# Kernel optimization log

Hardware: AMD Instinct MI355X
Metric: run time of the kernel (lower is better)

## Reference

```python
import jax, jax.numpy as jnp
import numpy as np

DIM = 128
NUM_SLOTS = 8
ITERS = 3
EPS = 1e-8
LN_EPS = 1e-3
HIDDEN = max(DIM, 128)


def _ln(x, w, b):
    mu = jnp.mean(x, axis=-1, keepdims=True)
    var = jnp.mean(jnp.square(x - mu), axis=-1, keepdims=True)
    return (x - mu) * jax.lax.rsqrt(var + LN_EPS) * w + b


def setup_inputs() -> dict:
    key = jax.random.key(0)
    ks = jax.random.split(key, 16)
    b, n, d, h = 32, 4096, DIM, HIDDEN
    limit = np.sqrt(6.0 / (1 + d))
    inp = {
        'inputs': jax.random.normal(ks[0], (b, n, d), jnp.float32),
        'slots_mu': jax.random.uniform(ks[1], (1, 1, d), jnp.float32, -limit, limit),
        'slots_log_sigma': jax.random.uniform(ks[2], (1, 1, d), jnp.float32, -limit, limit),
        'Wq': jax.random.normal(ks[3], (d, d), jnp.float32) / np.sqrt(d),
        'Wk': jax.random.normal(ks[4], (d, d), jnp.float32) / np.sqrt(d),
        'Wv': jax.random.normal(ks[5], (d, d), jnp.float32) / np.sqrt(d),
        'W_ih': jax.random.normal(ks[6], (3 * d, d), jnp.float32) / np.sqrt(d),
        'W_hh': jax.random.normal(ks[7], (3 * d, d), jnp.float32) / np.sqrt(d),
        'b_ih': jnp.zeros((3 * d,), jnp.float32),
        'b_hh': jnp.zeros((3 * d,), jnp.float32),
        'W1': jax.random.normal(ks[8], (h, d), jnp.float32) / np.sqrt(d),
        'b1': jnp.zeros((h,), jnp.float32),
        'W2': jax.random.normal(ks[9], (d, h), jnp.float32) / np.sqrt(h),
        'b2': jnp.zeros((d,), jnp.float32),
        'ln_in_w': jnp.ones((d,), jnp.float32), 'ln_in_b': jnp.zeros((d,), jnp.float32),
        'ln_s_w': jnp.ones((d,), jnp.float32), 'ln_s_b': jnp.zeros((d,), jnp.float32),
        'ln_ff_w': jnp.ones((d,), jnp.float32), 'ln_ff_b': jnp.zeros((d,), jnp.float32),
    }
    return inp


def reference(inputs, slots_mu, slots_log_sigma, Wq, Wk, Wv, W_ih, W_hh, b_ih, b_hh,
              W1, b1, W2, b2, ln_in_w, ln_in_b, ln_s_w, ln_s_b, ln_ff_w, ln_ff_b):
    b, n, d = inputs.shape
    scale = d ** -0.5
    # stochastic slot init (reparameterized, fixed key for determinism)
    noise = jax.random.normal(jax.random.key(42), (b, NUM_SLOTS, d), inputs.dtype)
    slots = slots_mu + jnp.exp(slots_log_sigma) * noise

    x = _ln(inputs, ln_in_w, ln_in_b)
    k = jnp.einsum('bnd,ed->bne', x, Wk)
    v = jnp.einsum('bnd,ed->bne', x, Wv)

    for _ in range(ITERS):
        slots_prev = slots
        q = jnp.einsum('bsd,ed->bse', _ln(slots, ln_s_w, ln_s_b), Wq)
        dots = jnp.einsum('bid,bjd->bij', q, k) * scale          # [b, slots, n]
        attn = jax.nn.softmax(dots, axis=1) + EPS                 # softmax over slots
        attn = attn / jnp.sum(attn, axis=-1, keepdims=True)       # normalize over tokens
        updates = jnp.einsum('bjd,bij->bid', v, attn)             # [b, slots, d]
        # GRUCell(updates, slots_prev)
        gx = jnp.einsum('bsd,ed->bse', updates, W_ih) + b_ih
        gh = jnp.einsum('bsd,ed->bse', slots_prev, W_hh) + b_hh
        xr, xz, xn = jnp.split(gx, 3, axis=-1)
        hr, hz, hn = jnp.split(gh, 3, axis=-1)
        r = jax.nn.sigmoid(xr + hr)
        z = jax.nn.sigmoid(xz + hz)
        ng = jnp.tanh(xn + r * hn)
        slots = (1.0 - z) * ng + z * slots_prev
        # residual MLP
        ff = _ln(slots, ln_ff_w, ln_ff_b)
        ff = jax.nn.relu(jnp.einsum('bsd,hd->bsh', ff, W1) + b1)
        slots = slots + jnp.einsum('bsh,dh->bsd', ff, W2) + b2
    return slots
```

## Files before the change

### kernel.cpp

```cpp
#include <hip/hip_runtime.h>
#include <hip/hip_bf16.h>
#include <math.h>

#define DIM 128
#define NSLOT 8
#define NTOK 4096
#define NB 32
#define CHUNK 128
#define NCH (NTOK / CHUNK)
#define CHUNKPAD 136
#define LN_EPS 1e-3f
#define ATT_EPS 1e-8f
#define SCALE 0.08838834764831845f

#define BM 64
#define LDK 136

typedef short bf16x8 __attribute__((ext_vector_type(8)));
typedef float f32x4 __attribute__((ext_vector_type(4)));
typedef unsigned short ushort8_t __attribute__((ext_vector_type(8)));

__device__ __forceinline__ float bf2f(unsigned short u) {
  return __uint_as_float(((unsigned)u) << 16);
}
__device__ __forceinline__ unsigned short f2bf(float f) {
  unsigned u = __float_as_uint(f);
  unsigned r = (u + 0x7FFFu + ((u >> 16) & 1u)) >> 16;
  return (unsigned short)r;
}

__device__ __forceinline__ float erfinv_like_xla(float x) {
  double xd = (double)x;
  double w = -log1p(-xd * xd);
  double p;
  if (w < 5.0) {
    w = w - 2.5;
    p = 2.81022636e-08;
    p = 3.43273939e-07 + p * w;
    p = -3.5233877e-06 + p * w;
    p = -4.39150654e-06 + p * w;
    p = 0.00021858087 + p * w;
    p = -0.00125372503 + p * w;
    p = -0.00417768164 + p * w;
    p = 0.246640727 + p * w;
    p = 1.50140941 + p * w;
  } else {
    w = sqrt(w) - 3.0;
    p = -0.000200214257;
    p = 0.000100950558 + p * w;
    p = 0.00134934322 + p * w;
    p = -0.00367342844 + p * w;
    p = 0.00573950773 + p * w;
    p = -0.0076224613 + p * w;
    p = 0.00943887047 + p * w;
    p = 1.00167406 + p * w;
    p = 2.83297682 + p * w;
  }
  return (float)(p * xd);
}

__global__ __launch_bounds__(256) void k_init_slots(
    const float* __restrict__ mu, const float* __restrict__ lsig,
    float* __restrict__ slots, const float* __restrict__ Wk,
    const float* __restrict__ Wv, unsigned short* __restrict__ Wbf) {
  int t = blockIdx.x * blockDim.x + threadIdx.x;
  if (t < DIM * DIM) {
    Wbf[t] = f2bf(Wk[t]);
    Wbf[DIM * DIM + t] = f2bf(Wv[t]);
  }
  if (t >= NB * NSLOT * DIM) return;
  uint32_t x0 = 0u, x1 = (uint32_t)t;
  uint32_t k0 = 0u, k1 = 42u;
  uint32_t ks[3] = {k0, k1, k0 ^ k1 ^ 0x1BD11BDAu};
  x0 += ks[0];
  x1 += ks[1];
  const int rot[2][4] = {{13, 15, 26, 6}, {17, 29, 16, 24}};
#pragma unroll
  for (int blk = 0; blk < 5; ++blk) {
    const int* r = rot[blk & 1];
#pragma unroll
    for (int j = 0; j < 4; ++j) {
      x0 += x1;
      x1 = (x1 << r[j]) | (x1 >> (32 - r[j]));
      x1 ^= x0;
    }
    x0 += ks[(blk + 1) % 3];
    x1 += ks[(blk + 2) % 3] + (uint32_t)(blk + 1);
  }
  uint32_t bits = x0 ^ x1;
  float f = __uint_as_float((bits >> 9) | 0x3F800000u) - 1.0f;
  const float mn = __uint_as_float(0xBF7FFFFFu);
  float u = fmaxf(f * 2.0f + mn, mn);
  float noise = 1.41421356f * erfinv_like_xla(u);
  int d = t & (DIM - 1);
  slots[t] = mu[d] + expf(lsig[d]) * noise;
}

__global__ __launch_bounds__(256) void k_ln_kv(
    const float* __restrict__ inp, const unsigned short* __restrict__ Wbf,
    const float* __restrict__ lnw, const float* __restrict__ lnb,
    unsigned short* __restrict__ kt, unsigned short* __restrict__ vt) {
  __shared__ __align__(16) unsigned short A[BM * LDK];
  __shared__ __align__(16) unsigned short Bv[DIM * 72];
  int t = threadIdx.x;
  int tg = blockIdx.x;

  {
    int r = t >> 2, qh = t & 3;
    const float* src = inp + ((size_t)tg * BM + r) * DIM + qh * 32;
    float xr[32];
    float s = 0.f, sq = 0.f;
#pragma unroll
    for (int i4 = 0; i4 < 8; ++i4) {
      float4 v = *reinterpret_cast<const float4*>(src + i4 * 4);
      xr[i4 * 4 + 0] = v.x; xr[i4 * 4 + 1] = v.y;
      xr[i4 * 4 + 2] = v.z; xr[i4 * 4 + 3] = v.w;
      s += v.x + v.y + v.z + v.w;
      sq += v.x * v.x + v.y * v.y + v.z * v.z + v.w * v.w;
    }
    s += __shfl_xor(s, 1); sq += __shfl_xor(sq, 1);
    s += __shfl_xor(s, 2); sq += __shfl_xor(sq, 2);
    float mean = s * (1.0f / DIM);
    float var = fmaxf(sq * (1.0f / DIM) - mean * mean, 0.0f);
    float inv = 1.0f / sqrtf(var + LN_EPS);
#pragma unroll
    for (int c8 = 0; c8 < 4; ++c8) {
      ushort8_t pk;
#pragma unroll
      for (int j = 0; j < 8; ++j) {
        int d = qh * 32 + c8 * 8 + j;
        float y = (xr[c8 * 8 + j] - mean) * inv * lnw[d] + lnb[d];
        pk[j] = f2bf(y);
      }
      *reinterpret_cast<ushort8_t*>(&A[r * LDK + qh * 32 + c8 * 8]) = pk;
    }
  }
  __syncthreads();

  int w = t >> 6, l = t & 63, lm = l & 15, lg = l >> 4;
  int mat = w >> 1;
  int ebase = (w & 1) * 64;
  const unsigned short* Wsrc = Wbf + mat * DIM * DIM;

  f32x4 acc[4][4];
#pragma unroll
  for (int i = 0; i < 4; ++i)
#pragma unroll
    for (int j = 0; j < 4; ++j) acc[i][j] = (f32x4){0.f, 0.f, 0.f, 0.f};

  if (mat == 0) {
#pragma unroll
    for (int ks = 0; ks < 4; ++ks) {
      bf16x8 wf[4], xf[4];
#pragma unroll
      for (int et = 0; et < 4; ++et)
        wf[et] = *reinterpret_cast<const bf16x8*>(
            Wsrc + (ebase + et * 16 + lm) * DIM + ks * 32 + 8 * lg);
#pragma unroll
      for (int tt = 0; tt < 4; ++tt)
        xf[tt] = *reinterpret_cast<const bf16x8*>(
            &A[(tt * 16 + lm) * LDK + ks * 32 + 8 * lg]);
#pragma unroll
      for (int tt = 0; tt < 4; ++tt)
#pragma unroll
        for (int et = 0; et < 4; ++et)
          acc[tt][et] = __builtin_amdgcn_mfma_f32_16x16x32_bf16(
              xf[tt], wf[et], acc[tt][et], 0, 0, 0);
    }
  } else {
#pragma unroll
    for (int ks = 0; ks < 4; ++ks) {
      bf16x8 wf[4], xf[4];
#pragma unroll
      for (int et = 0; et < 4; ++et)
        wf[et] = *reinterpret_cast<const bf16x8*>(
            Wsrc + (ebase + et * 16 + lm) * DIM + ks * 32 + 8 * lg);
#pragma unroll
      for (int tt = 0; tt < 4; ++tt)
        xf[tt] = *reinterpret_cast<const bf16x8*>(
            &A[(tt * 16 + lm) * LDK + ks * 32 + 8 * lg]);
#pragma unroll
      for (int et = 0; et < 4; ++et)
#pragma unroll
        for (int tt = 0; tt < 4; ++tt)
          acc[et][tt] = __builtin_amdgcn_mfma_f32_16x16x32_bf16(
              wf[et], xf[tt], acc[et][tt], 0, 0, 0);
    }
  }
  __syncthreads();

  if (mat == 0) {
#pragma unroll
    for (int tt = 0; tt < 4; ++tt)
#pragma unroll
      for (int et = 0; et < 4; ++et)
#pragma unroll
        for (int r = 0; r < 4; ++r)
          A[(tt * 16 + 4 * lg + r) * LDK + ebase + et * 16 + lm] =
              f2bf(acc[tt][et][r]);
  } else {
#pragma unroll
    for (int et = 0; et < 4; ++et)
#pragma unroll
      for (int tt = 0; tt < 4; ++tt)
#pragma unroll
        for (int r = 0; r < 4; ++r)
          Bv[(ebase + et * 16 + 4 * lg + r) * 72 + tt * 16 + lm] =
              f2bf(acc[et][tt][r]);
  }
  __syncthreads();

  {
    size_t rowbase = (size_t)tg * BM;
#pragma unroll
    for (int u = 0; u < 4; ++u) {
      int i = u * 256 + t;
      int tok = i >> 4, off = (i & 15) * 8;
      ushort8_t vv = *reinterpret_cast<const ushort8_t*>(&A[tok * LDK + off]);
      *reinterpret_cast<ushort8_t*>(&kt[(rowbase + tok) * DIM + off]) = vv;
    }
    int bb = tg >> 6;
    int nb = (tg & 63) * BM;
#pragma unroll
    for (int u = 0; u < 4; ++u) {
      int i = u * 256 + t;
      int e = i >> 3, off = (i & 7) * 8;
      ushort8_t vv = *reinterpret_cast<const ushort8_t*>(&Bv[e * 72 + off]);
      *reinterpret_cast<ushort8_t*>(
          &vt[((size_t)bb * DIM + e) * NTOK + nb + off]) = vv;
    }
  }
}

__global__ __launch_bounds__(256) void k_q0(
    const float* __restrict__ slots, const float* __restrict__ Wq,
    const float* __restrict__ lnw, const float* __restrict__ lnb,
    unsigned short* __restrict__ qbf) {
  int b = blockIdx.x, t = threadIdx.x;
  int s = t >> 5, c = t & 31;
  __shared__ __align__(16) float sln[NSLOT][DIM];
  const float* sb = slots + (b * NSLOT + s) * DIM;
  float4 xv = *reinterpret_cast<const float4*>(sb + c * 4);
  float ps = xv.x + xv.y + xv.z + xv.w;
  float pq = xv.x * xv.x + xv.y * xv.y + xv.z * xv.z + xv.w * xv.w;
#pragma unroll
  for (int m = 16; m >= 1; m >>= 1) {
    ps += __shfl_xor(ps, m, 32);
    pq += __shfl_xor(pq, m, 32);
  }
  float mean = ps * (1.0f / DIM);
  float var = fmaxf(pq * (1.0f / DIM) - mean * mean, 0.0f);
  float inv = 1.0f / sqrtf(var + LN_EPS);
  float vals[4] = {xv.x, xv.y, xv.z, xv.w};
#pragma unroll
  for (int ii = 0; ii < 4; ++ii) {
    int d = c * 4 + ii;
    sln[s][d] = (vals[ii] - mean) * inv * lnw[d] + lnb[d];
  }
  __syncthreads();
#pragma unroll
  for (int ii = 0; ii < 4; ++ii) {
    int e = c + 32 * ii;
    const float* wr = Wq + e * DIM;
    float acc = 0.0f;
#pragma unroll
    for (int d4 = 0; d4 < DIM / 4; ++d4) {
      float4 w4 = *reinterpret_cast<const float4*>(wr + d4 * 4);
      float4 s4 = *reinterpret_cast<const float4*>(&sln[s][d4 * 4]);
      acc += s4.x * w4.x + s4.y * w4.y + s4.z * w4.z + s4.w * w4.w;
    }
    qbf[(b * NSLOT + s) * DIM + e] = f2bf(SCALE * acc);
  }
}

__global__ __launch_bounds__(512, 4) void k_attn(
    const unsigned short* __restrict__ qbf, const unsigned short* __restrict__ kt,
    const unsigned short* __restrict__ vt, float* __restrict__ Np,
    float* __restrict__ Dp) {
  int bid = blockIdx.x;
  int b = bid >> 5, ch = bid & 31;
  int n0 = ch * CHUNK;
  int t = threadIdx.x;
  int wid = t >> 6, l = t & 63, lm = l & 15, lg = l >> 4;

  __shared__ __align__(16) unsigned short a_lds[NSLOT][CHUNKPAD];

  {
    const unsigned short* qb = qbf + (b * NSLOT + (lm & 7)) * DIM;
    bf16x8 aq[4];
#pragma unroll
    for (int ks = 0; ks < 4; ++ks)
      aq[ks] = *reinterpret_cast<const bf16x8*>(qb + ks * 32 + 8 * lg);
    const unsigned short* kb = kt + ((size_t)b * NTOK + n0) * DIM;
    int tok = wid * 16 + lm;
    f32x4 acc = (f32x4){0.f, 0.f, 0.f, 0.f};
#pragma unroll
    for (int ks = 0; ks < 4; ++ks) {
      bf16x8 bk = *reinterpret_cast<const bf16x8*>(
          kb + (size_t)tok * DIM + ks * 32 + 8 * lg);
      acc = __builtin_amdgcn_mfma_f32_16x16x32_bf16(aq[ks], bk, acc, 0, 0, 0);
    }
    float m4 = fmaxf(fmaxf(acc[0], acc[1]), fmaxf(acc[2], acc[3]));
    float m8 = fmaxf(m4, __shfl_xor(m4, 16));
    float e0 = expf(acc[0] - m8), e1 = expf(acc[1] - m8);
    float e2 = expf(acc[2] - m8), e3 = expf(acc[3] - m8);
    float s4 = e0 + e1 + e2 + e3;
    float s8 = s4 + __shfl_xor(s4, 16);
    float rs = 1.0f / s8;
    if (lg < 2) {
      a_lds[4 * lg + 0][tok] = f2bf(e0 * rs + ATT_EPS);
      a_lds[4 * lg + 1][tok] = f2bf(e1 * rs + ATT_EPS);
      a_lds[4 * lg + 2][tok] = f2bf(e2 * rs + ATT_EPS);
      a_lds[4 * lg + 3][tok] = f2bf(e3 * rs + ATT_EPS);
    }
  }
  __syncthreads();

  {
    float s = 0.0f;
#pragma unroll
    for (int jj = 0; jj < CHUNK / 64; ++jj) s += bf2f(a_lds[wid][l + 64 * jj]);
#pragma unroll
    for (int m = 32; m >= 1; m >>= 1) s += __shfl_xor(s, m);
    if (l == 0) Dp[(b * NCH + ch) * NSLOT + wid] = s;
  }

  {
    f32x4 acc = (f32x4){0.f, 0.f, 0.f, 0.f};
    const unsigned short* vb =
        vt + ((size_t)b * DIM + wid * 16 + lm) * NTOK + n0;
#pragma unroll
    for (int kk = 0; kk < CHUNK / 32; ++kk) {
      bf16x8 af = *reinterpret_cast<const bf16x8*>(
          &a_lds[lm & 7][kk * 32 + 8 * lg]);
      bf16x8 bv = *reinterpret_cast<const bf16x8*>(vb + kk * 32 + 8 * lg);
      acc = __builtin_amdgcn_mfma_f32_16x16x32_bf16(af, bv, acc, 0, 0, 0);
    }
    if (lg < 2) {
#pragma unroll
      for (int r = 0; r < 4; ++r)
        Np[((size_t)(b * NCH + ch) * NSLOT + 4 * lg + r) * DIM + wid * 16 +
           lm] = acc[r];
    }
  }
}

__global__ __launch_bounds__(256) void k_update(
    float* __restrict__ slots, unsigned short* __restrict__ qbf,
    const float* __restrict__ Np, const float* __restrict__ Dp,
    const float* __restrict__ W_ih, const float* __restrict__ W_hh,
    const float* __restrict__ b_ih, const float* __restrict__ b_hh,
    const float* __restrict__ W1, const float* __restrict__ b1,
    const float* __restrict__ W2, const float* __restrict__ b2,
    const float* __restrict__ lnfw, const float* __restrict__ lnfb,
    const float* __restrict__ Wq, const float* __restrict__ lnsw,
    const float* __restrict__ lnsb) {
  int bs = blockIdx.x;
  int b = bs >> 3, s = bs & 7;
  int t = threadIdx.x;
  __shared__ __align__(16) float upd[DIM];
  __shared__ __align__(16) float sprev[DIM];
  __shared__ __align__(16) float snew[DIM];
  __shared__ __align__(16) float ffin[DIM];
  __shared__ __align__(16) float ffb[DIM];
  __shared__ __align__(16) float gx[3 * DIM];
  __shared__ __align__(16) float gh[3 * DIM];

  float dsum = 0.0f;
  for (int ch = 0; ch < NCH; ++ch) dsum += Dp[(b * NCH + ch) * NSLOT + s];

  if (t < DIM) {
    sprev[t] = slots[(b * NSLOT + s) * DIM + t];
    float a = 0.0f;
    for (int ch = 0; ch < NCH; ++ch)
      a += Np[((size_t)(b * NCH + ch) * NSLOT + s) * DIM + t];
    upd[t] = a / dsum;
  }
  __syncthreads();

  for (int e = t; e < 3 * DIM; e += 256) {
    const float* wi = W_ih + e * DIM;
    const float* wh = W_hh + e * DIM;
    float ax = 0.0f, ah = 0.0f;
#pragma unroll
    for (int d4 = 0; d4 < DIM / 4; ++d4) {
      float4 u4 = *reinterpret_cast<const float4*>(&upd[d4 * 4]);
      float4 p4 = *reinterpret_cast<const float4*>(&sprev[d4 * 4]);
      float4 wi4 = *reinterpret_cast<const float4*>(wi + d4 * 4);
      float4 wh4 = *reinterpret_cast<const float4*>(wh + d4 * 4);
      ax += u4.x * wi4.x + u4.y * wi4.y + u4.z * wi4.z + u4.w * wi4.w;
      ah += p4.x * wh4.x + p4.y * wh4.y + p4.z * wh4.z + p4.w * wh4.w;
    }
    gx[e] = ax + b_ih[e];
    gh[e] = ah + b_hh[e];
  }
  __syncthreads();

  if (t < DIM) {
    float xr = gx[t], xz = gx[DIM + t], xn = gx[2 * DIM + t];
    float hr = gh[t], hz = gh[DIM + t], hn = gh[2 * DIM + t];
    float r = 1.0f / (1.0f + expf(-(xr + hr)));
    float z = 1.0f / (1.0f + expf(-(xz + hz)));
    float ng = tanhf(xn + r * hn);
    snew[t] = (1.0f - z) * ng + z * sprev[t];
  }
  __syncthreads();

  if (t < DIM) {
    float s1 = 0.0f, s2 = 0.0f;
#pragma unroll 8
    for (int d = 0; d < DIM; ++d) {
      float v = snew[d];
      s1 += v;
      s2 += v * v;
    }
    float mean = s1 * (1.0f / DIM);
    float var = fmaxf(s2 * (1.0f / DIM) - mean * mean, 0.0f);
    float inv = 1.0f / sqrtf(var + LN_EPS);
    ffin[t] = (snew[t] - mean) * inv * lnfw[t] + lnfb[t];
  }
  __syncthreads();

  if (t < DIM) {
    const float* wr = W1 + t * DIM;
    float acc = 0.0f;
#pragma unroll
    for (int d4 = 0; d4 < DIM / 4; ++d4) {
      float4 f4 = *reinterpret_cast<const float4*>(&ffin[d4 * 4]);
      float4 w4 = *reinterpret_cast<const float4*>(wr + d4 * 4);
      acc += f4.x * w4.x + f4.y * w4.y + f4.z * w4.z + f4.w * w4.w;
    }
    ffb[t] = fmaxf(acc + b1[t], 0.0f);
  }
  __syncthreads();

  if (t < DIM) {
    const float* wr = W2 + t * DIM;
    float acc = 0.0f;
#pragma unroll
    for (int h4 = 0; h4 < DIM / 4; ++h4) {
      float4 f4 = *reinterpret_cast<const float4*>(&ffb[h4 * 4]);
      float4 w4 = *reinterpret_cast<const float4*>(wr + h4 * 4);
      acc += f4.x * w4.x + f4.y * w4.y + f4.z * w4.z + f4.w * w4.w;
    }
    float val = snew[t] + acc + b2[t];
    slots[(b * NSLOT + s) * DIM + t] = val;
    gx[t] = val;
  }
  __syncthreads();

  if (t < DIM) {
    float s1 = 0.0f, s2 = 0.0f;
#pragma unroll 8
    for (int d = 0; d < DIM; ++d) {
      float v = gx[d];
      s1 += v;
      s2 += v * v;
    }
    float mean = s1 * (1.0f / DIM);
    float var = fmaxf(s2 * (1.0f / DIM) - mean * mean, 0.0f);
    float inv = 1.0f / sqrtf(var + LN_EPS);
    gh[t] = (gx[t] - mean) * inv * lnsw[t] + lnsb[t];
  }
  __syncthreads();

  if (t < DIM) {
    const float* wr = Wq + t * DIM;
    float acc = 0.0f;
#pragma unroll
    for (int d4 = 0; d4 < DIM / 4; ++d4) {
      float4 g4 = *reinterpret_cast<const float4*>(&gh[d4 * 4]);
      float4 w4 = *reinterpret_cast<const float4*>(wr + d4 * 4);
      acc += g4.x * w4.x + g4.y * w4.y + g4.z * w4.z + g4.w * w4.w;
    }
    qbf[(b * NSLOT + s) * DIM + t] = f2bf(SCALE * acc);
  }
}

__global__ __launch_bounds__(256) void k_sentinel(float* __restrict__ out,
                                                  int n) {
  int i = blockIdx.x * blockDim.x + threadIdx.x;
  if (i < n) out[i] = 1234.5f;
}

extern "C" void kernel_launch(void* const* d_in, const int* in_sizes, int n_in,
                              void* d_out, int out_size, void* d_ws,
                              size_t ws_size, hipStream_t stream) {
  const float* inp = (const float*)d_in[0];
  const float* mu = (const float*)d_in[1];
  const float* lsig = (const float*)d_in[2];
  const float* Wq = (const float*)d_in[3];
  const float* Wk = (const float*)d_in[4];
  const float* Wv = (const float*)d_in[5];
  const float* W_ih = (const float*)d_in[6];
  const float* W_hh = (const float*)d_in[7];
  const float* b_ih = (const float*)d_in[8];
  const float* b_hh = (const float*)d_in[9];
  const float* W1 = (const float*)d_in[10];
  const float* b1 = (const float*)d_in[11];
  const float* W2 = (const float*)d_in[12];
  const float* b2 = (const float*)d_in[13];
  const float* ln_in_w = (const float*)d_in[14];
  const float* ln_in_b = (const float*)d_in[15];
  const float* ln_s_w = (const float*)d_in[16];
  const float* ln_s_b = (const float*)d_in[17];
  const float* ln_ff_w = (const float*)d_in[18];
  const float* ln_ff_b = (const float*)d_in[19];

  float* slots = (float*)d_out;

  const size_t kv_elems = (size_t)NB * DIM * NTOK;
  const size_t np_elems = (size_t)NB * NCH * NSLOT * DIM;
  const size_t dp_elems = (size_t)NB * NCH * NSLOT;
  const size_t q_elems = (size_t)NB * NSLOT * DIM;
  size_t need = kv_elems * 2 * 2 + np_elems * 4 + dp_elems * 4 + q_elems * 2;
  if (ws_size < need) {
    k_sentinel<<<(out_size + 255) / 256, 256, 0, stream>>>((float*)d_out,
                                                           out_size);
    return;
  }
  char* wsb = (char*)d_ws;
  unsigned short* kt = (unsigned short*)wsb;
  unsigned short* vt = kt + kv_elems;
  float* Np = (float*)(wsb + kv_elems * 4);
  float* Dp = Np + np_elems;
  unsigned short* qbf = (unsigned short*)(Dp + dp_elems);
  unsigned short* Wbf = (unsigned short*)Np;

  k_init_slots<<<(NB * NSLOT * DIM) / 256, 256, 0, stream>>>(mu, lsig, slots,
                                                             Wk, Wv, Wbf);
  k_ln_kv<<<NB * NTOK / BM, 256, 0, stream>>>(inp, Wbf, ln_in_w, ln_in_b, kt,
                                              vt);
  k_q0<<<NB, 256, 0, stream>>>(slots, Wq, ln_s_w, ln_s_b, qbf);
  for (int it = 0; it < 3; ++it) {
    k_attn<<<NB * NCH, 512, 0, stream>>>(qbf, kt, vt, Np, Dp);
    k_update<<<NB * NSLOT, 256, 0, stream>>>(slots, qbf, Np, Dp, W_ih, W_hh,
                                             b_ih, b_hh, W1, b1, W2, b2,
                                             ln_ff_w, ln_ff_b, Wq, ln_s_w,
                                             ln_s_b);
  }
}
```

Measured before the change: 194.0 us.

## Fuse slot init with q0, widen LN/KV blocks to 512 threads, split Np reduction

Merges the slot-noise initialisation and the first query projection into one kernel per batch, which removes a launch. The LN+KV projection kernel now uses 512 threads per block, so each wave computes a 32-wide output slice and holds fewer accumulators, which raises occupancy. The update kernel splits the partial-numerator sum over chunks across all 256 threads instead of 128. The trade-off is that the fused init kernel has only 32 blocks doing serial work, so it can run longer than the two kernels it replaces.

```diff
diff --git a/kernel.cpp b/kernel.cpp
--- a/kernel.cpp
+++ b/kernel.cpp
@@ -62,41 +62,94 @@
 __global__ __launch_bounds__(256) void k_init_slots(
     const float* __restrict__ mu, const float* __restrict__ lsig,
     float* __restrict__ slots, const float* __restrict__ Wk,
-    const float* __restrict__ Wv, unsigned short* __restrict__ Wbf) {
-  int t = blockIdx.x * blockDim.x + threadIdx.x;
-  if (t < DIM * DIM) {
-    Wbf[t] = f2bf(Wk[t]);
-    Wbf[DIM * DIM + t] = f2bf(Wv[t]);
-  }
-  if (t >= NB * NSLOT * DIM) return;
-  uint32_t x0 = 0u, x1 = (uint32_t)t;
-  uint32_t k0 = 0u, k1 = 42u;
-  uint32_t ks[3] = {k0, k1, k0 ^ k1 ^ 0x1BD11BDAu};
-  x0 += ks[0];
-  x1 += ks[1];
-  const int rot[2][4] = {{13, 15, 26, 6}, {17, 29, 16, 24}};
-#pragma unroll
-  for (int blk = 0; blk < 5; ++blk) {
-    const int* r = rot[blk & 1];
-#pragma unroll
-    for (int j = 0; j < 4; ++j) {
-      x0 += x1;
-      x1 = (x1 << r[j]) | (x1 >> (32 - r[j]));
-      x1 ^= x0;
-    }
-    x0 += ks[(blk + 1) % 3];
-    x1 += ks[(blk + 2) % 3] + (uint32_t)(blk + 1);
-  }
-  uint32_t bits = x0 ^ x1;
-  float f = __uint_as_float((bits >> 9) | 0x3F800000u) - 1.0f;
-  const float mn = __uint_as_float(0xBF7FFFFFu);
-  float u = fmaxf(f * 2.0f + mn, mn);
-  float noise = 1.41421356f * erfinv_like_xla(u);
-  int d = t & (DIM - 1);
-  slots[t] = mu[d] + expf(lsig[d]) * noise;
-}
-
-__global__ __launch_bounds__(256) void k_ln_kv(
+    const float* __restrict__ Wv, unsigned short* __restrict__ Wbf,
+    const float* __restrict__ Wq, const float* __restrict__ lnw,
+    const float* __restrict__ lnb, unsigned short* __restrict__ qbf) {
+  int b = blockIdx.x, t = threadIdx.x;
+  __shared__ __align__(16) float sc[NSLOT][DIM];
+  __shared__ __align__(16) float sln[NSLOT][DIM];
+
+#pragma unroll
+  for (int u = 0; u < 2; ++u) {
+    int i = b * 512 + u * 256 + t;
+    Wbf[i] = f2bf(Wk[i]);
+    Wbf[DIM * DIM + i] = f2bf(Wv[i]);
+  }
+
+#pragma unroll
+  for (int r4 = 0; r4 < 4; ++r4) {
+    int idx = b * 1024 + r4 * 256 + t;
+    uint32_t x0 = 0u, x1 = (uint32_t)idx;
+    uint32_t k0 = 0u, k1 = 42u;
+    uint32_t ks[3] = {k0, k1, k0 ^ k1 ^ 0x1BD11BDAu};
+    x0 += ks[0];
+    x1 += ks[1];
+    const int rot[2][4] = {{13, 15, 26, 6}, {17, 29, 16, 24}};
+#pragma unroll
+    for (int blk = 0; blk < 5; ++blk) {
+      const int* r = rot[blk & 1];
+#pragma unroll
+      for (int j = 0; j < 4; ++j) {
+        x0 += x1;
+        x1 = (x1 << r[j]) | (x1 >> (32 - r[j]));
+        x1 ^= x0;
+      }
+      x0 += ks[(blk + 1) % 3];
+      x1 += ks[(blk + 2) % 3] + (uint32_t)(blk + 1);
+    }
+    uint32_t bits = x0 ^ x1;
+    float f = __uint_as_float((bits >> 9) | 0x3F800000u) - 1.0f;
+    const float mn = __uint_as_float(0xBF7FFFFFu);
+    float u = fmaxf(f * 2.0f + mn, mn);
+    float noise = 1.41421356f * erfinv_like_xla(u);
+    int d = idx & (DIM - 1);
+    float val = mu[d] + expf(lsig[d]) * noise;
+    slots[idx] = val;
+    int li = r4 * 256 + t;
+    sc[li >> 7][li & (DIM - 1)] = val;
+  }
+  __syncthreads();
+
+  {
+    int s = t >> 5, c = t & 31;
+    float4 xv = *reinterpret_cast<const float4*>(&sc[s][c * 4]);
+    float ps = xv.x + xv.y + xv.z + xv.w;
+    float pq = xv.x * xv.x + xv.y * xv.y + xv.z * xv.z + xv.w * xv.w;
+#pragma unroll
+    for (int m = 16; m >= 1; m >>= 1) {
+      ps += __shfl_xor(ps, m, 32);
+      pq += __shfl_xor(pq, m, 32);
+    }
+    float mean = ps * (1.0f / DIM);
+    float var = fmaxf(pq * (1.0f / DIM) - mean * mean, 0.0f);
+    float inv = 1.0f / sqrtf(var + LN_EPS);
+    float vals[4] = {xv.x, xv.y, xv.z, xv.w};
+#pragma unroll
+    for (int ii = 0; ii < 4; ++ii) {
+      int d = c * 4 + ii;
+      sln[s][d] = (vals[ii] - mean) * inv * lnw[d] + lnb[d];
+    }
+  }
+  __syncthreads();
+  {
+    int s = t >> 5, c = t & 31;
+#pragma unroll
+    for (int ii = 0; ii < 4; ++ii) {
+      int e = c + 32 * ii;
+      const float* wr = Wq + e * DIM;
+      float acc = 0.0f;
+#pragma unroll
+      for (int d4 = 0; d4 < DIM / 4; ++d4) {
+        float4 w4 = *reinterpret_cast<const float4*>(wr + d4 * 4);
+        float4 s4 = *reinterpret_cast<const float4*>(&sln[s][d4 * 4]);
+        acc += s4.x * w4.x + s4.y * w4.y + s4.z * w4.z + s4.w * w4.w;
+      }
+      qbf[(b * NSLOT + s) * DIM + e] = f2bf(SCALE * acc);
+    }
+  }
+}
+
+__global__ __launch_bounds__(512) void k_ln_kv(
     const float* __restrict__ inp, const unsigned short* __restrict__ Wbf,
     const float* __restrict__ lnw, const float* __restrict__ lnb,
     unsigned short* __restrict__ kt, unsigned short* __restrict__ vt) {
@@ -106,12 +159,12 @@
   int tg = blockIdx.x;
 
   {
-    int r = t >> 2, qh = t & 3;
-    const float* src = inp + ((size_t)tg * BM + r) * DIM + qh * 32;
-    float xr[32];
+    int r = t >> 3, p = t & 7;
+    const float* src = inp + ((size_t)tg * BM + r) * DIM + p * 16;
+    float xr[16];
     float s = 0.f, sq = 0.f;
 #pragma unroll
-    for (int i4 = 0; i4 < 8; ++i4) {
+    for (int i4 = 0; i4 < 4; ++i4) {
       float4 v = *reinterpret_cast<const float4*>(src + i4 * 4);
       xr[i4 * 4 + 0] = v.x; xr[i4 * 4 + 1] = v.y;
       xr[i4 * 4 + 2] = v.z; xr[i4 * 4 + 3] = v.w;
@@ -120,40 +173,39 @@
     }
     s += __shfl_xor(s, 1); sq += __shfl_xor(sq, 1);
     s += __shfl_xor(s, 2); sq += __shfl_xor(sq, 2);
+    s += __shfl_xor(s, 4); sq += __shfl_xor(sq, 4);
     float mean = s * (1.0f / DIM);
     float var = fmaxf(sq * (1.0f / DIM) - mean * mean, 0.0f);
     float inv = 1.0f / sqrtf(var + LN_EPS);
 #pragma unroll
-    for (int c8 = 0; c8 < 4; ++c8) {
+    for (int c8 = 0; c8 < 2; ++c8) {
       ushort8_t pk;
 #pragma unroll
       for (int j = 0; j < 8; ++j) {
-        int d = qh * 32 + c8 * 8 + j;
+        int d = p * 16 + c8 * 8 + j;
         float y = (xr[c8 * 8 + j] - mean) * inv * lnw[d] + lnb[d];
         pk[j] = f2bf(y);
       }
-      *reinterpret_cast<ushort8_t*>(&A[r * LDK + qh * 32 + c8 * 8]) = pk;
+      *reinterpret_cast<ushort8_t*>(&A[r * LDK + p * 16 + c8 * 8]) = pk;
     }
   }
   __syncthreads();
 
   int w = t >> 6, l = t & 63, lm = l & 15, lg = l >> 4;
-  int mat = w >> 1;
-  int ebase = (w & 1) * 64;
+  int mat = w >> 2;
+  int ebase = (w & 3) * 32;
   const unsigned short* Wsrc = Wbf + mat * DIM * DIM;
 
-  f32x4 acc[4][4];
-#pragma unroll
-  for (int i = 0; i < 4; ++i)
-#pragma unroll
-    for (int j = 0; j < 4; ++j) acc[i][j] = (f32x4){0.f, 0.f, 0.f, 0.f};
+  f32x4 acc[8];
+#pragma unroll
+  for (int i = 0; i < 8; ++i) acc[i] = (f32x4){0.f, 0.f, 0.f, 0.f};
 
   if (mat == 0) {
 #pragma unroll
     for (int ks = 0; ks < 4; ++ks) {
-      bf16x8 wf[4], xf[4];
-#pragma unroll
-      for (int et = 0; et < 4; ++et)
+      bf16x8 wf[2], xf[4];
+#pragma unroll
+      for (int et = 0; et < 2; ++et)
         wf[et] = *reinterpret_cast<const bf16x8*>(
             Wsrc + (ebase + et * 16 + lm) * DIM + ks * 32 + 8 * lg);
 #pragma unroll
@@ -163,16 +215,16 @@
 #pragma unroll
       for (int tt = 0; tt < 4; ++tt)
 #pragma unroll
-        for (int et = 0; et < 4; ++et)
-          acc[tt][et] = __builtin_amdgcn_mfma_f32_16x16x32_bf16(
-              xf[tt], wf[et], acc[tt][et], 0, 0, 0);
+        for (int et = 0; et < 2; ++et)
+          acc[tt * 2 + et] = __builtin_amdgcn_mfma_f32_16x16x32_bf16(
+              xf[tt], wf[et], acc[tt * 2 + et], 0, 0, 0);
     }
   } else {
 #pragma unroll
     for (int ks = 0; ks < 4; ++ks) {
-      bf16x8 wf[4], xf[4];
-#pragma unroll
-      for (int et = 0; et < 4; ++et)
+      bf16x8 wf[2], xf[4];
+#pragma unroll
+      for (int et = 0; et < 2; ++et)
         wf[et] = *reinterpret_cast<const bf16x8*>(
             Wsrc + (ebase + et * 16 + lm) * DIM + ks * 32 + 8 * lg);
 #pragma unroll
@@ -180,11 +232,11 @@
         xf[tt] = *reinterpret_cast<const bf16x8*>(
             &A[(tt * 16 + lm) * LDK + ks * 32 + 8 * lg]);
 #pragma unroll
-      for (int et = 0; et < 4; ++et)
+      for (int et = 0; et < 2; ++et)
 #pragma unroll
         for (int tt = 0; tt < 4; ++tt)
-          acc[et][tt] = __builtin_amdgcn_mfma_f32_16x16x32_bf16(
-              wf[et], xf[tt], acc[et][tt], 0, 0, 0);
+          acc[et * 4 + tt] = __builtin_amdgcn_mfma_f32_16x16x32_bf16(
+              wf[et], xf[tt], acc[et * 4 + tt], 0, 0, 0);
     }
   }
   __syncthreads();
@@ -193,28 +245,28 @@
 #pragma unroll
     for (int tt = 0; tt < 4; ++tt)
 #pragma unroll
-      for (int et = 0; et < 4; ++et)
+      for (int et = 0; et < 2; ++et)
 #pragma unroll
         for (int r = 0; r < 4; ++r)
           A[(tt * 16 + 4 * lg + r) * LDK + ebase + et * 16 + lm] =
-              f2bf(acc[tt][et][r]);
+              f2bf(acc[tt * 2 + et][r]);
   } else {
 #pragma unroll
-    for (int et = 0; et < 4; ++et)
+    for (int et = 0; et < 2; ++et)
 #pragma unroll
       for (int tt = 0; tt < 4; ++tt)
 #pragma unroll
         for (int r = 0; r < 4; ++r)
           Bv[(ebase + et * 16 + 4 * lg + r) * 72 + tt * 16 + lm] =
-              f2bf(acc[et][tt][r]);
+              f2bf(acc[et * 4 + tt][r]);
   }
   __syncthreads();
 
   {
     size_t rowbase = (size_t)tg * BM;
 #pragma unroll
-    for (int u = 0; u < 4; ++u) {
-      int i = u * 256 + t;
+    for (int u = 0; u < 2; ++u) {
+      int i = u * 512 + t;
       int tok = i >> 4, off = (i & 15) * 8;
       ushort8_t vv = *reinterpret_cast<const ushort8_t*>(&A[tok * LDK + off]);
       *reinterpret_cast<ushort8_t*>(&kt[(rowbase + tok) * DIM + off]) = vv;
@@ -222,54 +274,13 @@
     int bb = tg >> 6;
     int nb = (tg & 63) * BM;
 #pragma unroll
-    for (int u = 0; u < 4; ++u) {
-      int i = u * 256 + t;
+    for (int u = 0; u < 2; ++u) {
+      int i = u * 512 + t;
       int e = i >> 3, off = (i & 7) * 8;
       ushort8_t vv = *reinterpret_cast<const ushort8_t*>(&Bv[e * 72 + off]);
       *reinterpret_cast<ushort8_t*>(
           &vt[((size_t)bb * DIM + e) * NTOK + nb + off]) = vv;
     }
-  }
-}
-
-__global__ __launch_bounds__(256) void k_q0(
-    const float* __restrict__ slots, const float* __restrict__ Wq,
-    const float* __restrict__ lnw, const float* __restrict__ lnb,
-    unsigned short* __restrict__ qbf) {
-  int b = blockIdx.x, t = threadIdx.x;
-  int s = t >> 5, c = t & 31;
-  __shared__ __align__(16) float sln[NSLOT][DIM];
-  const float* sb = slots + (b * NSLOT + s) * DIM;
-  float4 xv = *reinterpret_cast<const float4*>(sb + c * 4);
-  float ps = xv.x + xv.y + xv.z + xv.w;
-  float pq = xv.x * xv.x + xv.y * xv.y + xv.z * xv.z + xv.w * xv.w;
-#pragma unroll
-  for (int m = 16; m >= 1; m >>= 1) {
-    ps += __shfl_xor(ps, m, 32);
-    pq += __shfl_xor(pq, m, 32);
-  }
-  float mean = ps * (1.0f / DIM);
-  float var = fmaxf(pq * (1.0f / DIM) - mean * mean, 0.0f);
-  float inv = 1.0f / sqrtf(var + LN_EPS);
-  float vals[4] = {xv.x, xv.y, xv.z, xv.w};
-#pragma unroll
-  for (int ii = 0; ii < 4; ++ii) {
-    int d = c * 4 + ii;
-    sln[s][d] = (vals[ii] - mean) * inv * lnw[d] + lnb[d];
-  }
-  __syncthreads();
-#pragma unroll
-  for (int ii = 0; ii < 4; ++ii) {
-    int e = c + 32 * ii;
-    const float* wr = Wq + e * DIM;
-    float acc = 0.0f;
-#pragma unroll
-    for (int d4 = 0; d4 < DIM / 4; ++d4) {
-      float4 w4 = *reinterpret_cast<const float4*>(wr + d4 * 4);
-      float4 s4 = *reinterpret_cast<const float4*>(&sln[s][d4 * 4]);
-      acc += s4.x * w4.x + s4.y * w4.y + s4.z * w4.z + s4.w * w4.w;
-    }
-    qbf[(b * NSLOT + s) * DIM + e] = f2bf(SCALE * acc);
   }
 }
 
@@ -358,6 +369,7 @@
   int bs = blockIdx.x;
   int b = bs >> 3, s = bs & 7;
   int t = threadIdx.x;
+  __shared__ __align__(16) float pn[2][DIM];
   __shared__ __align__(16) float upd[DIM];
   __shared__ __align__(16) float sprev[DIM];
   __shared__ __align__(16) float snew[DIM];
@@ -369,13 +381,16 @@
   float dsum = 0.0f;
   for (int ch = 0; ch < NCH; ++ch) dsum += Dp[(b * NCH + ch) * NSLOT + s];
 
-  if (t < DIM) {
-    sprev[t] = slots[(b * NSLOT + s) * DIM + t];
+  {
+    int d = t & (DIM - 1), h = t >> 7;
     float a = 0.0f;
-    for (int ch = 0; ch < NCH; ++ch)
-      a += Np[((size_t)(b * NCH + ch) * NSLOT + s) * DIM + t];
-    upd[t] = a / dsum;
-  }
+    for (int ch = h * (NCH / 2); ch < (h + 1) * (NCH / 2); ++ch)
+      a += Np[((size_t)(b * NCH + ch) * NSLOT + s) * DIM + d];
+    pn[h][d] = a;
+    if (h == 0) sprev[d] = slots[(b * NSLOT + s) * DIM + d];
+  }
+  __syncthreads();
+  if (t < DIM) upd[t] = (pn[0][t] + pn[1][t]) / dsum;
   __syncthreads();
 
   for (int e = t; e < 3 * DIM; e += 256) {
@@ -527,11 +542,10 @@
   unsigned short* qbf = (unsigned short*)(Dp + dp_elems);
   unsigned short* Wbf = (unsigned short*)Np;
 
-  k_init_slots<<<(NB * NSLOT * DIM) / 256, 256, 0, stream>>>(mu, lsig, slots,
-                                                             Wk, Wv, Wbf);
-  k_ln_kv<<<NB * NTOK / BM, 256, 0, stream>>>(inp, Wbf, ln_in_w, ln_in_b, kt,
+  k_init_slots<<<NB, 256, 0, stream>>>(mu, lsig, slots, Wk, Wv, Wbf, Wq,
+                                       ln_s_w, ln_s_b, qbf);
+  k_ln_kv<<<NB * NTOK / BM, 512, 0, stream>>>(inp, Wbf, ln_in_w, ln_in_b, kt,
                                               vt);
-  k_q0<<<NB, 256, 0, stream>>>(slots, Wq, ln_s_w, ln_s_b, qbf);
   for (int it = 0; it < 3; ++it) {
     k_attn<<<NB * NCH, 512, 0, stream>>>(qbf, kt, vt, Np, Dp);
     k_update<<<NB * NSLOT, 256, 0, stream>>>(slots, qbf, Np, Dp, W_ih, W_hh,
```

Result: faster. 185.8 us (-4.3%).
